# Performance work log

Measured on AMD Instinct MI355X. Metric: run time of the kernel, lower is better.

The kernel has to match this reference:

```python
import jax, jax.numpy as jnp
import numpy as np

N_ITER = 50  # default n_iter in entmax_bisect
ALPHA_START, ALPHA_END, SCHED_STEPS = 1.0, 1.5, 10000


def entmax_bisect(x, alpha, n_iter=N_ITER):
    """Faithful port of entmax_bisect (Peters & Martins) forward, alpha-entmax over last dim."""
    d = x.shape[-1]
    am1 = alpha - 1.0
    pow_inv = 1.0 / am1  # 1/(alpha-1); =2 for alpha=1.5
    Xs = x * am1
    max_val = jnp.max(Xs, axis=-1, keepdims=True)
    tau_lo = max_val - 1.0                    # _gp(1, alpha) = 1^(alpha-1) = 1
    tau_hi = max_val - (1.0 / d) ** am1       # _gp(1/d, alpha)
    f_lo = jnp.sum(jnp.clip(Xs - tau_lo, 0.0) ** pow_inv, axis=-1, keepdims=True) - 1.0
    dm0 = tau_hi - tau_lo

    def body(i, carry):
        tau_lo, dm, _ = carry
        dm = dm * 0.5
        tau_m = tau_lo + dm
        p_m = jnp.clip(Xs - tau_m, 0.0) ** pow_inv
        f_m = jnp.sum(p_m, axis=-1, keepdims=True) - 1.0
        tau_lo = jnp.where(f_m * f_lo >= 0.0, tau_m, tau_lo)
        return (tau_lo, dm, p_m)

    p0 = jnp.zeros_like(Xs)
    _, _, p_m = jax.lax.fori_loop(0, n_iter, body, (tau_lo, dm0, p0))
    # ensure_sum_one=True
    return p_m / jnp.sum(p_m, axis=-1, keepdims=True)


def setup_inputs() -> dict:
    key = jax.random.key(0)
    x = jax.random.normal(key, (8, 16, 1024, 1024), dtype=jnp.float32)
    return {"x": x, "step": 10000}


def reference(x, step):
    t = min(step, SCHED_STEPS) / SCHED_STEPS
    alpha = ALPHA_START + t * (ALPHA_END - ALPHA_START)  # 1.5 at step=10000
    return entmax_bisect(x, alpha)
```

## Files before the change

### kernel.cpp

```cpp
#include <hip/hip_runtime.h>


#define D 1024
#define N_ITER 30
#define K1 5

typedef float v2f __attribute__((ext_vector_type(2)));

__global__ __launch_bounds__(256) void entmax15_kernel(const float* __restrict__ x,
                                                       float* __restrict__ out) {
    const int lane = threadIdx.x & 63;
    const int wave = threadIdx.x >> 6;
    const long long row = (long long)blockIdx.x * 4 + wave;

    const float4* __restrict__ xr  = (const float4*)(x + row * D);
    float4* __restrict__       orr = (float4*)(out + row * D);

    __shared__ float sv_lds[4][128];

    const v2f zero2 = (v2f){0.0f, 0.0f};

    v2f xs[8];
#pragma unroll
    for (int j = 0; j < 4; ++j) {
        float4 v = xr[lane + 64 * j];
        xs[2 * j + 0] = (v2f){v.x, v.y} * 0.5f;
        xs[2 * j + 1] = (v2f){v.z, v.w} * 0.5f;
    }

    v2f m2 = xs[0];
#pragma unroll
    for (int e = 1; e < 8; ++e) m2 = __builtin_elementwise_max(m2, xs[e]);
    float m = fmaxf(m2.x, m2.y);
#pragma unroll
    for (int off = 32; off >= 1; off >>= 1) m = fmaxf(m, __shfl_xor(m, off, 64));

    float tau_lo = m - 1.0f;
    float dm = 0.96875f;
    float tau_m = tau_lo;
    float s = 1.0f;

#pragma unroll 1
    for (int it = 0; it < K1; ++it) {
        dm *= 0.5f;
        tau_m = tau_lo + dm;
        const v2f tm2 = (v2f){tau_m, tau_m};
        v2f acc = zero2;
#pragma unroll
        for (int e = 0; e < 8; ++e) {
            v2f t = __builtin_elementwise_max(xs[e] - tm2, zero2);
            acc += t * t;
        }
        float f = acc.x + acc.y;
#pragma unroll
        for (int off = 32; off >= 1; off >>= 1) f += __shfl_xor(f, off, 64);
        s = f;
        if (f >= 1.0f) tau_lo = tau_m;
    }

    const float cut = tau_lo;
    const unsigned long long lt = (lane == 0) ? 0ull : (~0ull >> (64 - lane));
    int base = 0;
#pragma unroll
    for (int e = 0; e < 16; ++e) {
        const float v = (e & 1) ? xs[e >> 1].y : xs[e >> 1].x;
        const unsigned long long mask = __ballot(v > cut);
        if (v > cut) {
            const int idx = base + (int)__popcll(mask & lt);
            if (idx < 128) sv_lds[wave][idx] = v;
        }
        base += (int)__popcll(mask);
    }
    const int S = base;

    __syncthreads();

    if (S <= 128) {
        float a0 = sv_lds[wave][lane];
        float a1 = sv_lds[wave][lane + 64];
        v2f sv;
        sv.x = (lane < S) ? a0 : -3.0e38f;
        sv.y = (lane + 64 < S) ? a1 : -3.0e38f;
#pragma unroll 1
        for (int it = K1; it < N_ITER; ++it) {
            dm *= 0.5f;
            tau_m = tau_lo + dm;
            const v2f tm2 = (v2f){tau_m, tau_m};
            v2f t = __builtin_elementwise_max(sv - tm2, zero2);
            v2f a = t * t;
            float f = a.x + a.y;
#pragma unroll
            for (int off = 32; off >= 1; off >>= 1) f += __shfl_xor(f, off, 64);
            s = f;
            if (f >= 1.0f) tau_lo = tau_m;
        }
    } else {
#pragma unroll 1
        for (int it = K1; it < N_ITER; ++it) {
            dm *= 0.5f;
            tau_m = tau_lo + dm;
            const v2f tm2 = (v2f){tau_m, tau_m};
            v2f acc = zero2;
#pragma unroll
            for (int e = 0; e < 8; ++e) {
                v2f t = __builtin_elementwise_max(xs[e] - tm2, zero2);
                acc += t * t;
            }
            float f = acc.x + acc.y;
#pragma unroll
            for (int off = 32; off >= 1; off >>= 1) f += __shfl_xor(f, off, 64);
            s = f;
            if (f >= 1.0f) tau_lo = tau_m;
        }
    }

    const float inv = 1.0f / s;
    const v2f tm2 = (v2f){tau_m, tau_m};
    const v2f inv2 = (v2f){inv, inv};
#pragma unroll
    for (int j = 0; j < 4; ++j) {
        v2f a = __builtin_elementwise_max(xs[2 * j + 0] - tm2, zero2);
        v2f b = __builtin_elementwise_max(xs[2 * j + 1] - tm2, zero2);
        a = a * a * inv2;
        b = b * b * inv2;
        float4 v;
        v.x = a.x; v.y = a.y; v.z = b.x; v.w = b.y;
        orr[lane + 64 * j] = v;
    }
}

extern "C" void kernel_launch(void* const* d_in, const int* in_sizes, int n_in,
                              void* d_out, int out_size, void* d_ws, size_t ws_size,
                              hipStream_t stream) {
    const float* x = (const float*)d_in[0];
    float* out = (float*)d_out;
    const long long n_rows = (long long)out_size / D;
    const int blocks = (int)(n_rows / 4);
    entmax15_kernel<<<blocks, 256, 0, stream>>>(x, out);
}
```

Baseline: 890.8 us.

## Replace bisection threshold search with Newton iterations on compacted support

```diff
diff --git a/kernel.cpp b/kernel.cpp
--- a/kernel.cpp
+++ b/kernel.cpp
@@ -2,10 +2,33 @@
 
 
 #define D 1024
-#define N_ITER 30
-#define K1 5
+#define NFULL 2
+#define NCOMP 9
 
 typedef float v2f __attribute__((ext_vector_type(2)));
+
+__device__ __forceinline__ void wave_reduce2(float& a, float& b) {
+#pragma unroll
+    for (int off = 32; off >= 1; off >>= 1) {
+        a += __shfl_xor(a, off, 64);
+        b += __shfl_xor(b, off, 64);
+    }
+}
+
+__device__ __forceinline__ void eval_full(const v2f* xs, float tau, float& f, float& g) {
+    const v2f zero2 = (v2f){0.f, 0.f};
+    const v2f t2 = (v2f){tau, tau};
+    v2f accf = zero2, accg = zero2;
+#pragma unroll
+    for (int e = 0; e < 8; ++e) {
+        v2f t = __builtin_elementwise_max(xs[e] - t2, zero2);
+        accf += t * t;
+        accg += t;
+    }
+    f = accf.x + accf.y;
+    g = accg.x + accg.y;
+    wave_reduce2(f, g);
+}
 
 __global__ __launch_bounds__(256) void entmax15_kernel(const float* __restrict__ x,
                                                        float* __restrict__ out) {
@@ -17,8 +40,7 @@
     float4* __restrict__       orr = (float4*)(out + row * D);
 
     __shared__ float sv_lds[4][128];
-
-    const v2f zero2 = (v2f){0.0f, 0.0f};
+    const v2f zero2 = (v2f){0.f, 0.f};
 
     v2f xs[8];
 #pragma unroll
@@ -35,87 +57,59 @@
 #pragma unroll
     for (int off = 32; off >= 1; off >>= 1) m = fmaxf(m, __shfl_xor(m, off, 64));
 
-    float tau_lo = m - 1.0f;
-    float dm = 0.96875f;
-    float tau_m = tau_lo;
-    float s = 1.0f;
-
-#pragma unroll 1
-    for (int it = 0; it < K1; ++it) {
-        dm *= 0.5f;
-        tau_m = tau_lo + dm;
-        const v2f tm2 = (v2f){tau_m, tau_m};
-        v2f acc = zero2;
+    float tau = m - 1.0f;
+    float f, g;
+    eval_full(xs, tau, f, g);
 #pragma unroll
-        for (int e = 0; e < 8; ++e) {
-            v2f t = __builtin_elementwise_max(xs[e] - tm2, zero2);
-            acc += t * t;
-        }
-        float f = acc.x + acc.y;
-#pragma unroll
-        for (int off = 32; off >= 1; off >>= 1) f += __shfl_xor(f, off, 64);
-        s = f;
-        if (f >= 1.0f) tau_lo = tau_m;
+    for (int it = 0; it < NFULL; ++it) {
+        tau += (f - 1.0f) * __builtin_amdgcn_rcpf(2.0f * g);
+        eval_full(xs, tau, f, g);
     }
 
-    const float cut = tau_lo;
+    const float cut = tau;
     const unsigned long long lt = (lane == 0) ? 0ull : (~0ull >> (64 - lane));
     int base = 0;
 #pragma unroll
     for (int e = 0; e < 16; ++e) {
         const float v = (e & 1) ? xs[e >> 1].y : xs[e >> 1].x;
-        const unsigned long long mask = __ballot(v > cut);
+        const unsigned long long mk = __ballot(v > cut);
         if (v > cut) {
-            const int idx = base + (int)__popcll(mask & lt);
+            const int idx = base + (int)__popcll(mk & lt);
             if (idx < 128) sv_lds[wave][idx] = v;
         }
-        base += (int)__popcll(mask);
+        base += (int)__popcll(mk);
     }
     const int S = base;
 
     __syncthreads();
 
     if (S <= 128) {
-        float a0 = sv_lds[wave][lane];
-        float a1 = sv_lds[wave][lane + 64];
         v2f sv;
-        sv.x = (lane < S) ? a0 : -3.0e38f;
-        sv.y = (lane + 64 < S) ? a1 : -3.0e38f;
+        {
+            float a0 = sv_lds[wave][lane];
+            float a1 = sv_lds[wave][lane + 64];
+            sv.x = (lane < S) ? a0 : -1.0e30f;
+            sv.y = (lane + 64 < S) ? a1 : -1.0e30f;
+        }
 #pragma unroll 1
-        for (int it = K1; it < N_ITER; ++it) {
-            dm *= 0.5f;
-            tau_m = tau_lo + dm;
-            const v2f tm2 = (v2f){tau_m, tau_m};
-            v2f t = __builtin_elementwise_max(sv - tm2, zero2);
-            v2f a = t * t;
-            float f = a.x + a.y;
-#pragma unroll
-            for (int off = 32; off >= 1; off >>= 1) f += __shfl_xor(f, off, 64);
-            s = f;
-            if (f >= 1.0f) tau_lo = tau_m;
+        for (int it = 0; it < NCOMP; ++it) {
+            tau += (f - 1.0f) * __builtin_amdgcn_rcpf(2.0f * g);
+            v2f t = __builtin_elementwise_max(sv - (v2f){tau, tau}, zero2);
+            v2f ff = t * t;
+            f = ff.x + ff.y;
+            g = t.x + t.y;
+            wave_reduce2(f, g);
         }
     } else {
 #pragma unroll 1
-        for (int it = K1; it < N_ITER; ++it) {
-            dm *= 0.5f;
-            tau_m = tau_lo + dm;
-            const v2f tm2 = (v2f){tau_m, tau_m};
-            v2f acc = zero2;
-#pragma unroll
-            for (int e = 0; e < 8; ++e) {
-                v2f t = __builtin_elementwise_max(xs[e] - tm2, zero2);
-                acc += t * t;
-            }
-            float f = acc.x + acc.y;
-#pragma unroll
-            for (int off = 32; off >= 1; off >>= 1) f += __shfl_xor(f, off, 64);
-            s = f;
-            if (f >= 1.0f) tau_lo = tau_m;
+        for (int it = 0; it < NCOMP; ++it) {
+            tau += (f - 1.0f) * __builtin_amdgcn_rcpf(2.0f * g);
+            eval_full(xs, tau, f, g);
         }
     }
 
-    const float inv = 1.0f / s;
-    const v2f tm2 = (v2f){tau_m, tau_m};
+    const float inv = 1.0f / f;
+    const v2f tm2 = (v2f){tau, tau};
     const v2f inv2 = (v2f){inv, inv};
 #pragma unroll
     for (int j = 0; j < 4; ++j) {
```

Measured after the change: 861.3 us. 3.3% less time.
